# Kernel optimization log

Measured on AMD Instinct MI355X. Metric: run time of the kernel, lower is better.

## Reference

```python
import jax, jax.numpy as jnp
import numpy as np

V, T_BLOCK, D, H, L, HS = 32000, 1024, 1024, 16, 6, 64
B, T = 4, 1024
EPS = 1e-5


def setup_inputs() -> dict:
    key = jax.random.key(0)
    ks = jax.random.split(key, 12)
    s = 0.02  # init std, matches _init_weights
    return {
        'input_tokens': jax.random.randint(ks[0], (B, T), 0, V),
        'tok_emb': jax.random.normal(ks[1], (V, D), jnp.float32) * s,
        'pos_emb': jax.random.normal(ks[2], (T_BLOCK, D), jnp.float32) * s,
        'Wq': jax.random.normal(ks[3], (L, H, D, HS), jnp.float32) * s,
        'Wk': jax.random.normal(ks[4], (L, H, D, HS), jnp.float32) * s,
        'Wv': jax.random.normal(ks[5], (L, H, D, HS), jnp.float32) * s,
        'Wo': jax.random.normal(ks[6], (L, D, D), jnp.float32) * s,
        'bo': jnp.zeros((L, D), jnp.float32),
        'ln1_g': jnp.ones((L, D), jnp.float32),
        'ln1_b': jnp.zeros((L, D), jnp.float32),
        'ln2_g': jnp.ones((L, D), jnp.float32),
        'ln2_b': jnp.zeros((L, D), jnp.float32),
        'W1': jax.random.normal(ks[7], (L, D, 4 * D), jnp.float32) * s,
        'b1': jnp.zeros((L, 4 * D), jnp.float32),
        'W2': jax.random.normal(ks[8], (L, 4 * D, D), jnp.float32) * s,
        'b2': jnp.zeros((L, D), jnp.float32),
        'lnf_g': jnp.ones((D,), jnp.float32),
        'lnf_b': jnp.zeros((D,), jnp.float32),
        'W_out': jax.random.normal(ks[9], (D, V), jnp.float32) * s,
        'b_out': jnp.zeros((V,), jnp.float32),
    }


def _layer_norm(x, g, b):
    mu = jnp.mean(x, axis=-1, keepdims=True)
    var = jnp.mean(jnp.square(x - mu), axis=-1, keepdims=True)
    return (x - mu) * jax.lax.rsqrt(var + EPS) * g + b


def _attn(x, Wq, Wk, Wv, Wo, bo, causal_mask):
    # x: [B,T,D]; Wq/Wk/Wv: [H,D,hs] (per-head linears, bias=False)
    q = jnp.einsum('btd,hds->bhts', x, Wq)
    k = jnp.einsum('btd,hds->bhts', x, Wk)
    v = jnp.einsum('btd,hds->bhts', x, Wv)
    scores = jnp.einsum('bhts,bhus->bhtu', q, k) * (HS ** -0.5)
    scores = jnp.where(causal_mask, scores, -jnp.inf)
    w = jax.nn.softmax(scores, axis=-1)  # dropout=0.0 -> identity
    o = jnp.einsum('bhtu,bhus->bhts', w, v)
    # concat heads in order, then projection
    o = o.transpose(0, 2, 1, 3).reshape(x.shape[0], x.shape[1], H * HS)
    return o @ Wo + bo


def reference(input_tokens, tok_emb, pos_emb, Wq, Wk, Wv, Wo, bo,
              ln1_g, ln1_b, ln2_g, ln2_b, W1, b1, W2, b2,
              lnf_g, lnf_b, W_out, b_out):
    Bc, Tc = input_tokens.shape
    x = tok_emb[input_tokens] + pos_emb[:Tc]  # [B,T,D]
    mask = jnp.tril(jnp.ones((Tc, Tc), bool))[None, None]  # [1,1,T,T]
    for l in range(L):
        x = x + _attn(_layer_norm(x, ln1_g[l], ln1_b[l]),
                      Wq[l], Wk[l], Wv[l], Wo[l], bo[l], mask)
        h = _layer_norm(x, ln2_g[l], ln2_b[l])
        x = x + jax.nn.relu(h @ W1[l] + b1[l]) @ W2[l] + b2[l]
    x = _layer_norm(x, lnf_g, lnf_b)
    logits = x @ W_out + b_out  # [B,T,V]
    return logits
```

## Files before the change

kernel.cpp:

```cpp
#include <hip/hip_runtime.h>
#include <hip/hip_bf16.h>

#define HS 64
#define NH 16
#define DMODEL 1024
#define SEQ 1024
#define NB 4
#define NL 6
#define VOCAB 32000
#define EPS_LN 1e-5f

static constexpr int ROWS = NB * SEQ;

typedef float f32x4 __attribute__((ext_vector_type(4)));
typedef short bf16x8 __attribute__((ext_vector_type(8)));
typedef unsigned short u16x8 __attribute__((ext_vector_type(8)));
typedef unsigned short u16x4 __attribute__((ext_vector_type(4)));

__device__ __forceinline__ unsigned short f2b(float f) {
  __hip_bfloat16 h = __float2bfloat16(f);
  return *reinterpret_cast<unsigned short*>(&h);
}
__device__ __forceinline__ void gload_lds16(const void* g, void* l) {
  __builtin_amdgcn_global_load_lds(
      (const __attribute__((address_space(1))) void*)g,
      (__attribute__((address_space(3))) void*)l, 16, 0, 0);
}
#define MFMA16 __builtin_amdgcn_mfma_f32_16x16x32_bf16
#define EXP2F __builtin_amdgcn_exp2f

__global__ __launch_bounds__(256) void embed_kernel(
    const int* __restrict__ tokens, const float* __restrict__ tok_emb,
    const float* __restrict__ pos_emb, float* __restrict__ x) {
  int row = blockIdx.x;
  int t = row & (SEQ - 1);
  int tok = tokens[row];
  int d = threadIdx.x * 4;
  float4 te = *(const float4*)(tok_emb + (size_t)tok * DMODEL + d);
  float4 pe = *(const float4*)(pos_emb + (size_t)t * DMODEL + d);
  te.x += pe.x; te.y += pe.y; te.z += pe.z; te.w += pe.w;
  *(float4*)(x + (size_t)row * DMODEL + d) = te;
}

__global__ __launch_bounds__(256) void ln_kernel(
    const float* __restrict__ in, unsigned short* __restrict__ outp,
    const float* __restrict__ g, const float* __restrict__ b) {
  int row = blockIdx.x;
  int tid = threadIdx.x;
  const float* xr = in + (size_t)row * DMODEL;
  float4 v4 = *(const float4*)(xr + tid * 4);
  float s = v4.x + v4.y + v4.z + v4.w;
  float s2 = v4.x * v4.x + v4.y * v4.y + v4.z * v4.z + v4.w * v4.w;
#pragma unroll
  for (int off = 32; off > 0; off >>= 1) {
    s  += __shfl_down(s, off, 64);
    s2 += __shfl_down(s2, off, 64);
  }
  __shared__ float red[8];
  __shared__ float stats[2];
  int wv = tid >> 6, lane = tid & 63;
  if (lane == 0) { red[wv] = s; red[4 + wv] = s2; }
  __syncthreads();
  if (tid == 0) {
    float ts = red[0] + red[1] + red[2] + red[3];
    float ts2 = red[4] + red[5] + red[6] + red[7];
    float mu = ts * (1.0f / DMODEL);
    float var = ts2 * (1.0f / DMODEL) - mu * mu;
    stats[0] = mu;
    stats[1] = rsqrtf(var + EPS_LN);
  }
  __syncthreads();
  float mu = stats[0], rstd = stats[1];
  float4 g4 = *(const float4*)(g + tid * 4);
  float4 b4 = *(const float4*)(b + tid * 4);
  u16x4 o;
  o[0] = f2b((v4.x - mu) * rstd * g4.x + b4.x);
  o[1] = f2b((v4.y - mu) * rstd * g4.y + b4.y);
  o[2] = f2b((v4.z - mu) * rstd * g4.z + b4.z);
  o[3] = f2b((v4.w - mu) * rstd * g4.w + b4.w);
  *(u16x4*)(outp + (size_t)row * DMODEL + tid * 4) = o;
}

__global__ __launch_bounds__(256) void transconv(
    const float* __restrict__ in, unsigned short* __restrict__ outp, int K, int N) {
  __shared__ float tile[64][33];
  size_t zoff = (size_t)blockIdx.z * K * N;
  in += zoff;
  outp += zoff;
  int n0 = blockIdx.x * 32, k0 = blockIdx.y * 64;
  int tx = threadIdx.x & 31, ty = threadIdx.x >> 5;
#pragma unroll
  for (int i = 0; i < 8; ++i)
    tile[ty + i * 8][tx] = in[(size_t)(k0 + ty + i * 8) * N + n0 + tx];
  __syncthreads();
  int n = threadIdx.x >> 3;
  int kq = (threadIdx.x & 7) * 8;
  u16x8 o8;
#pragma unroll
  for (int j = 0; j < 8; ++j) o8[j] = f2b(tile[kq + j][n]);
  *(u16x8*)(outp + (size_t)(n0 + n) * K + k0 + kq) = o8;
}

__global__ __launch_bounds__(256) void qkv_transconv(
    const float* __restrict__ Wq, const float* __restrict__ Wk,
    const float* __restrict__ Wv, unsigned short* __restrict__ outp) {
  __shared__ float tile[64][33];
  int z = blockIdx.z;
  int l = z / 48;
  int r = z % 48;
  int which = r >> 4, h = r & 15;
  const float* W = (which == 0 ? Wq : which == 1 ? Wk : Wv) +
                   ((size_t)l * NH + h) * DMODEL * HS;
  int s0 = blockIdx.x * 32, d0 = blockIdx.y * 64;
  int tx = threadIdx.x & 31, ty = threadIdx.x >> 5;
#pragma unroll
  for (int i = 0; i < 8; ++i)
    tile[ty + i * 8][tx] = W[(size_t)(d0 + ty + i * 8) * HS + s0 + tx];
  __syncthreads();
  unsigned short* ob = outp + ((size_t)l * 3072 + which * 1024 + h * 64) * DMODEL;
  int n = threadIdx.x >> 3;
  int kq = (threadIdx.x & 7) * 8;
  u16x8 o8;
#pragma unroll
  for (int j = 0; j < 8; ++j) o8[j] = f2b(tile[kq + j][n]);
  *(u16x8*)(ob + (size_t)(s0 + n) * DMODEL + d0 + kq) = o8;
}

#define EPI_LOGITS 0
#define EPI_RES 1
#define EPI_RELU 2
#define EPI_QKV 3

template <int EPI, int BM_>
__global__ __launch_bounds__(512, 2) void mmX(
    const unsigned short* __restrict__ A, const unsigned short* __restrict__ Bt,
    const float* __restrict__ bias, const float* __restrict__ res,
    float* __restrict__ outf, unsigned short* __restrict__ ob0,
    unsigned short* __restrict__ ob1, unsigned short* __restrict__ ob2,
    int M, int N, int K) {
  constexpr int NA = BM_ / 64;
  constexpr int AP = BM_ / 128;
  constexpr int MFRAG = BM_ / 32;
  __shared__ __align__(16) unsigned short LDS[2][(BM_ + 256) * 64];
  const int tid = threadIdx.x;
  const int lane = tid & 63, w = tid >> 6;
  const int wm2 = w >> 2, wn4 = w & 3;
  const int l15 = lane & 15, l4 = lane >> 4;

  const int nM = M / BM_, nN = N >> 8;
  const int nwg = nM * nN;
  int bid = blockIdx.x;
  int wg = (bid & 7) * (nwg >> 3) + (bid >> 3);
  int mb = wg % nM, nb = wg / nM;
  const int m0 = mb * BM_, n0 = nb * 256;

  const int srow = tid >> 3;
  const int scolb = (tid & 7) * 16;
  const int swst = (srow & 7) << 4;
  const char* aS = (const char*)A + ((size_t)(m0 + srow) * K) * 2 + (scolb ^ swst);
  const char* bS = (const char*)Bt + ((size_t)(n0 + srow) * K) * 2 + (scolb ^ swst);
  const size_t rstep = (size_t)64 * K * 2;

  const int kb0 = l4 * 16;
  const int swz = (l15 & 7) << 4;

  const int NT = K >> 6;
  f32x4 acc[MFRAG][4] = {};
  bf16x8 bv[4][2], avA[AP][2], avB[AP][2];

#define STAGEX(tt)                                                          \
  {                                                                         \
    unsigned short* ad = &LDS[(tt) & 1][0] + (size_t)tid * 8;               \
    unsigned short* bd = &LDS[(tt) & 1][BM_ * 64] + (size_t)tid * 8;        \
    size_t ko = (size_t)(tt) * 128;                                         \
    _Pragma("unroll")                                                       \
    for (int j = 0; j < NA; ++j) gload_lds16(aS + ko + j * rstep, ad + j * 4096); \
    _Pragma("unroll")                                                       \
    for (int j = 0; j < 4; ++j) gload_lds16(bS + ko + j * rstep, bd + j * 4096);  \
  }

#define READA(dst, p)                                                       \
  _Pragma("unroll")                                                         \
  for (int mm = 0; mm < AP; ++mm)                                           \
  _Pragma("unroll")                                                         \
    for (int ks = 0; ks < 2; ++ks)                                          \
      dst[mm][ks] = *(const bf16x8*)(ab + (AP * (p) + mm) * 2048 +          \
                                     ((kb0 + 64 * ks) ^ swz));

#define GROUP(src, p)                                                       \
  __builtin_amdgcn_s_setprio(1);                                            \
  _Pragma("unroll")                                                         \
  for (int ks = 0; ks < 2; ++ks)                                            \
  _Pragma("unroll")                                                         \
    for (int mm = 0; mm < AP; ++mm)                                         \
    _Pragma("unroll")                                                       \
      for (int ni = 0; ni < 4; ++ni)                                        \
        acc[AP * (p) + mm][ni] =                                            \
            MFMA16(src[mm][ks], bv[ni][ks], acc[AP * (p) + mm][ni], 0, 0, 0);\
  __builtin_amdgcn_s_setprio(0);

  STAGEX(0)
  STAGEX(1)

  for (int t = 0; t < NT; ++t) {
    if (t < NT - 1) {
      if constexpr (BM_ == 256) asm volatile("s_waitcnt vmcnt(8)" ::: "memory");
      else                      asm volatile("s_waitcnt vmcnt(6)" ::: "memory");
    } else {
      asm volatile("s_waitcnt vmcnt(0)" ::: "memory");
    }
    __builtin_amdgcn_s_barrier();
    __builtin_amdgcn_sched_barrier(0);
    const char* ab = (const char*)&LDS[t & 1][0] +
                     (size_t)(wm2 * (BM_ / 2) + l15) * 128;
    const char* bb = (const char*)&LDS[t & 1][BM_ * 64] +
                     (size_t)(wn4 * 64 + l15) * 128;
#pragma unroll
    for (int ni = 0; ni < 4; ++ni)
#pragma unroll
      for (int ks = 0; ks < 2; ++ks)
        bv[ni][ks] = *(const bf16x8*)(bb + ni * 2048 + ((kb0 + 64 * ks) ^ swz));
    READA(avA, 0)
    READA(avB, 1)
    GROUP(avA, 0)
    READA(avA, 2)
    GROUP(avB, 1)
    READA(avB, 3)
    GROUP(avA, 2)
    asm volatile("s_waitcnt lgkmcnt(0)" ::: "memory");
    __builtin_amdgcn_sched_barrier(0);
    __builtin_amdgcn_s_barrier();
    __builtin_amdgcn_sched_barrier(0);
    if (t + 2 < NT) STAGEX(t + 2)
    GROUP(avB, 3)
  }
#undef STAGEX
#undef READA
#undef GROUP

  int rbase = m0 + wm2 * (BM_ / 2) + (l4 << 2);
  int cbase = n0 + wn4 * 64 + l15;

  if constexpr (EPI == EPI_LOGITS) {
    float* fl = (float*)&LDS[0][0];
#pragma unroll
    for (int half = 0; half < 2; ++half) {
      __syncthreads();
      if (wm2 == half) {
#pragma unroll
        for (int ni = 0; ni < 4; ++ni) {
          float bvv = bias[cbase + ni * 16];
          int cl = wn4 * 64 + l15 + ni * 16;
#pragma unroll
          for (int mi = 0; mi < MFRAG; ++mi) {
            int rl = mi * 16 + (l4 << 2);
#pragma unroll
            for (int r = 0; r < 4; ++r)
              fl[(rl + r) * 256 + cl] = acc[mi][ni][r] + bvv;
          }
        }
      }
      __syncthreads();
#pragma unroll
      for (int j = 0; j < 16; ++j) {
        int idx = j * 512 + tid;
        int rl = idx >> 6;
        int cc = (idx & 63) << 2;
        f32x4 v4 = *(const f32x4*)&fl[rl * 256 + cc];
        float* gp = outf + (size_t)(m0 + half * 128 + rl) * N + n0 + cc;
        __builtin_nontemporal_store(v4, (f32x4*)gp);
      }
    }
  } else {
#pragma unroll
    for (int ni = 0; ni < 4; ++ni) {
      int col = cbase + ni * 16;
      float bvv = 0.f;
      if (EPI != EPI_QKV) bvv = bias[col];
      if (EPI == EPI_QKV) {
        int which = col >> 10;
        int c2 = col & 1023;
        int h = c2 >> 6, s = c2 & 63;
#pragma unroll
        for (int mi = 0; mi < MFRAG; ++mi) {
          f32x4 a4 = acc[mi][ni];
          int row0 = rbase + mi * 16;
          int bb2 = row0 >> 10, t0 = row0 & 1023;
          if (which == 2) {
            u16x4 pk;
            pk[0] = f2b(a4[0]); pk[1] = f2b(a4[1]); pk[2] = f2b(a4[2]); pk[3] = f2b(a4[3]);
            *(u16x4*)(ob2 + ((((size_t)bb2 * NH + h) * HS) + s) * SEQ + t0) = pk;
          } else {
            unsigned short* dst = (which == 0) ? ob0 : ob1;
#pragma unroll
            for (int r = 0; r < 4; ++r)
              dst[((((size_t)bb2 * NH) + h) * SEQ + t0 + r) * HS + s] = f2b(a4[r]);
          }
        }
      } else {
#pragma unroll
        for (int mi = 0; mi < MFRAG; ++mi) {
          f32x4 a4 = acc[mi][ni];
#pragma unroll
          for (int r = 0; r < 4; ++r) {
            int rowg = rbase + mi * 16 + r;
            size_t off = (size_t)rowg * N + col;
            float v = a4[r] + bvv;
            if (EPI == EPI_RES) outf[off] = v + res[off];
            else if (EPI == EPI_RELU) ob0[off] = f2b(fmaxf(v, 0.f));
          }
        }
      }
    }
  }
}

template <int EPI>
__global__ __launch_bounds__(256, 2) void mmP(
    const unsigned short* __restrict__ A, const unsigned short* __restrict__ Bt,
    const float* __restrict__ bias, const float* __restrict__ res,
    float* __restrict__ outf, unsigned short* __restrict__ ob0,
    int M, int N, int K) {
  __shared__ __align__(16) unsigned short LDS[2][16384];
  const int tid = threadIdx.x;
  const int lane = tid & 63, w = tid >> 6;
  const int wm2 = w >> 1, wn2 = w & 1;
  const int l15 = lane & 15, l4 = lane >> 4;

  const int nM = M >> 7, nN = N >> 7;
  const int nwg = nM * nN;
  int bid = blockIdx.x;
  int wg = (bid & 7) * (nwg >> 3) + (bid >> 3);
  int mb = wg % nM, nb = wg / nM;
  const int m0 = mb * 128, n0 = nb * 128;

  const int srow = tid >> 3;
  const int scolb = (tid & 7) * 16;
  const int swst = (srow & 7) << 4;
  const char* aS = (const char*)A + ((size_t)(m0 + srow) * K) * 2 + (scolb ^ swst);
  const char* bS = (const char*)Bt + ((size_t)(n0 + srow) * K) * 2 + (scolb ^ swst);
  const size_t rstep = (size_t)32 * K * 2;

  const int kb0 = l4 * 16;
  const int swz = (l15 & 7) << 4;

  const int NT = K >> 6;
  f32x4 acc[4][4] = {};
  bf16x8 bv[4][2];

#define STAGEX(tt)                                                          \
  {                                                                         \
    unsigned short* ad = &LDS[(tt) & 1][0] + (size_t)tid * 8;               \
    unsigned short* bd = &LDS[(tt) & 1][8192] + (size_t)tid * 8;            \
    size_t ko = (size_t)(tt) * 128;                                         \
    _Pragma("unroll")                                                       \
    for (int j = 0; j < 4; ++j) gload_lds16(aS + ko + j * rstep, ad + j * 2048); \
    _Pragma("unroll")                                                       \
    for (int j = 0; j < 4; ++j) gload_lds16(bS + ko + j * rstep, bd + j * 2048); \
  }

#define RDA(dst, mi)                                                        \
  dst##k0 = *(const bf16x8*)(ab + (mi) * 2048 + (kb0 ^ swz));               \
  dst##k1 = *(const bf16x8*)(ab + (mi) * 2048 + ((kb0 + 64) ^ swz));

#define GROUP(src, mi)                                                      \
  __builtin_amdgcn_s_setprio(1);                                            \
  _Pragma("unroll")                                                         \
  for (int ni = 0; ni < 4; ++ni)                                            \
    acc[mi][ni] = MFMA16(src##k0, bv[ni][0], acc[mi][ni], 0, 0, 0);         \
  _Pragma("unroll")                                                         \
  for (int ni = 0; ni < 4; ++ni)                                            \
    acc[mi][ni] = MFMA16(src##k1, bv[ni][1], acc[mi][ni], 0, 0, 0);         \
  __builtin_amdgcn_s_setprio(0);

  STAGEX(0)
  STAGEX(1)

  for (int t = 0; t < NT; ++t) {
    if (t < NT - 1) asm volatile("s_waitcnt vmcnt(8)" ::: "memory");
    else            asm volatile("s_waitcnt vmcnt(0)" ::: "memory");
    __builtin_amdgcn_s_barrier();
    __builtin_amdgcn_sched_barrier(0);
    const char* ab = (const char*)&LDS[t & 1][0] + (size_t)(wm2 * 64 + l15) * 128;
    const char* bb = (const char*)&LDS[t & 1][8192] + (size_t)(wn2 * 64 + l15) * 128;
    bf16x8 aEk0, aEk1, aOk0, aOk1;
#pragma unroll
    for (int ni = 0; ni < 4; ++ni) {
      bv[ni][0] = *(const bf16x8*)(bb + ni * 2048 + (kb0 ^ swz));
      bv[ni][1] = *(const bf16x8*)(bb + ni * 2048 + ((kb0 + 64) ^ swz));
    }
    RDA(aE, 0)
    GROUP(aE, 0)
    RDA(aO, 1)
    GROUP(aO, 1)
    RDA(aE, 2)
    GROUP(aE, 2)
    RDA(aO, 3)
    asm volatile("s_waitcnt lgkmcnt(0)" ::: "memory");
    __builtin_amdgcn_sched_barrier(0);
    __builtin_amdgcn_s_barrier();
    __builtin_amdgcn_sched_barrier(0);
    if (t + 2 < NT) STAGEX(t + 2)
    GROUP(aO, 3)
  }
#undef STAGEX
#undef RDA
#undef GROUP

  int rbase = m0 + wm2 * 64 + (l4 << 2);
  int cbase = n0 + wn2 * 64 + l15;
#pragma unroll
  for (int ni = 0; ni < 4; ++ni) {
    int col = cbase + ni * 16;
    float bvv = bias[col];
#pragma unroll
    for (int mi = 0; mi < 4; ++mi) {
      f32x4 a4 = acc[mi][ni];
#pragma unroll
      for (int r = 0; r < 4; ++r) {
        int rowg = rbase + mi * 16 + r;
        size_t off = (size_t)rowg * N + col;
        float v = a4[r] + bvv;
        if (EPI == EPI_RES) outf[off] = v + res[off];
        else if (EPI == EPI_RELU) ob0[off] = f2b(fmaxf(v, 0.f));
      }
    }
  }
}

__global__ __launch_bounds__(256) void attn_mfma(
    const unsigned short* __restrict__ q, const unsigned short* __restrict__ k,
    const unsigned short* __restrict__ vt, unsigned short* __restrict__ outp) {
  __shared__ __align__(16) unsigned short S[32768];
  unsigned short* Ks = S;
  unsigned short* Vs = S + 16384;
  int qt = blockIdx.x, bh = blockIdx.y;
  int tid = threadIdx.x;
  int lane = tid & 63, w = tid >> 6;
  int l15 = lane & 15, l4 = lane >> 4;

  const unsigned short* qb = q + (size_t)bh * SEQ * HS;
  const unsigned short* kb = k + (size_t)bh * SEQ * HS;
  const unsigned short* vb = vt + (size_t)bh * HS * SEQ;

  int q_l = w * 16 + l15;
  int q_g = qt * 64 + q_l;
  bf16x8 qf[2];
  qf[0] = *(const bf16x8*)(qb + (size_t)q_g * HS + l4 * 8);
  qf[1] = *(const bf16x8*)(qb + (size_t)q_g * HS + l4 * 8 + 32);

  int kOff[4], vOff[4];
#pragma unroll
  for (int j = 0; j < 4; ++j) {
    int idx = tid + j * 256;
    kOff[j] = (idx >> 7) * 16 * HS + (idx & 15) * HS + ((idx >> 4) & 7) * 8;
    vOff[j] = ((idx >> 8) * 16 + (idx & 15)) * SEQ + ((idx >> 4) & 15) * 8;
  }

#define ASTAGE(tt)                                                           \
  {                                                                          \
    int bsel = ((tt) & 1) * 8192;                                            \
    const unsigned short* ksrc = kb + (size_t)(tt) * 128 * HS;               \
    const unsigned short* vsrc = vb + (tt) * 128;                            \
    _Pragma("unroll")                                                        \
    for (int j = 0; j < 4; ++j)                                              \
      gload_lds16(ksrc + kOff[j], Ks + bsel + (size_t)(tid + j * 256) * 8);  \
    _Pragma("unroll")                                                        \
    for (int j = 0; j < 4; ++j)                                              \
      gload_lds16(vsrc + vOff[j], Vs + bsel + (size_t)(tid + j * 256) * 8);  \
  }

  f32x4 o[4] = {};
  float mrun = -3e38f, lrun = 0.f;
  int baseLane = 32 * (l4 & 1) + l15;
  bool hi_t = (l4 >> 1) != 0;
  const float CSC = 0.125f * 1.44269504f;
  const float THR = 8.0f / CSC;

  int nt2 = (qt + 2) >> 1;
  ASTAGE(0)

  for (int kt = 0; kt < nt2; ++kt) {
    asm volatile("s_waitcnt vmcnt(0)" ::: "memory");
    __builtin_amdgcn_s_barrier();
    __builtin_amdgcn_sched_barrier(0);
    if (kt + 1 < nt2) ASTAGE(kt + 1)
    const unsigned short* Kb = Ks + (kt & 1) * 8192;
    const unsigned short* Vb = Vs + (kt & 1) * 8192;

    f32x4 s[8];
#pragma unroll
    for (int t = 0; t < 8; ++t) {
      bf16x8 kf0 = *(const bf16x8*)(Kb + ((size_t)(t * 8 + l4) * 16 + l15) * 8);
      bf16x8 kf1 = *(const bf16x8*)(Kb + ((size_t)(t * 8 + l4 + 4) * 16 + l15) * 8);
      s[t] = (f32x4){0.f, 0.f, 0.f, 0.f};
      s[t] = MFMA16(kf0, qf[0], s[t], 0, 0, 0);
      s[t] = MFMA16(kf1, qf[1], s[t], 0, 0, 0);
    }

    if (kt == nt2 - 1) {
      int keybase = kt * 128 + 4 * l4;
#pragma unroll
      for (int t = 0; t < 8; ++t)
#pragma unroll
        for (int r = 0; r < 4; ++r)
          if (keybase + 16 * t + r > q_g) s[t][r] = -3e38f;
    }
    float mx = -3e38f;
#pragma unroll
    for (int t = 0; t < 8; ++t)
#pragma unroll
      for (int r = 0; r < 4; ++r) mx = fmaxf(mx, s[t][r]);
    mx = fmaxf(mx, __shfl_xor(mx, 16, 64));
    mx = fmaxf(mx, __shfl_xor(mx, 32, 64));
    if (!__all(mx - mrun <= THR)) {
      float mnew = fmaxf(mrun, mx);
      float sc = EXP2F((mrun - mnew) * CSC);
      lrun *= sc;
#pragma unroll
      for (int t2 = 0; t2 < 4; ++t2)
#pragma unroll
        for (int r = 0; r < 4; ++r) o[t2][r] *= sc;
      mrun = mnew;
    }
    float mc = mrun * CSC;
    float ps = 0.f;
#pragma unroll
    for (int t = 0; t < 8; ++t)
#pragma unroll
      for (int r = 0; r < 4; ++r) {
        float e = EXP2F(__builtin_fmaf(s[t][r], CSC, -mc));
        s[t][r] = e;
        ps += e;
      }
    ps += __shfl_xor(ps, 16, 64);
    ps += __shfl_xor(ps, 32, 64);
    lrun += ps;

    int pd[8][2];
#pragma unroll
    for (int t = 0; t < 8; ++t)
#pragma unroll
      for (int h = 0; h < 2; ++h)
        pd[t][h] = (int)f2b(s[t][2 * h]) | ((int)f2b(s[t][2 * h + 1]) << 16);

#pragma unroll
    for (int kk = 0; kk < 4; ++kk) {
      int a0 = __shfl(pd[2 * kk][0], baseLane, 64);
      int b0 = __shfl(pd[2 * kk + 1][0], baseLane, 64);
      int a1 = __shfl(pd[2 * kk][1], baseLane, 64);
      int b1 = __shfl(pd[2 * kk + 1][1], baseLane, 64);
      int a2 = __shfl(pd[2 * kk][0], baseLane + 16, 64);
      int b2 = __shfl(pd[2 * kk + 1][0], baseLane + 16, 64);
      int a3 = __shfl(pd[2 * kk][1], baseLane + 16, 64);
      int b3 = __shfl(pd[2 * kk + 1][1], baseLane + 16, 64);
      union { int4 i4; bf16x8 v; } yu;
      yu.i4.x = hi_t ? b0 : a0;
      yu.i4.y = hi_t ? b1 : a1;
      yu.i4.z = hi_t ? b2 : a2;
      yu.i4.w = hi_t ? b3 : a3;
#pragma unroll
      for (int t2 = 0; t2 < 4; ++t2) {
        bf16x8 vf = *(const bf16x8*)(Vb + ((size_t)(t2 * 16 + kk * 4 + l4) * 16 + l15) * 8);
        o[t2] = MFMA16(vf, yu.v, o[t2], 0, 0, 0);
      }
    }
  }
#undef ASTAGE

  __syncthreads();
  float inv = 1.0f / lrun;
  unsigned short* Ol = S;
#pragma unroll
  for (int t2 = 0; t2 < 4; ++t2) {
    u16x4 p4;
#pragma unroll
    for (int r = 0; r < 4; ++r) p4[r] = f2b(o[t2][r] * inv);
    *(u16x4*)(Ol + (size_t)q_l * 72 + 16 * t2 + 4 * l4) = p4;
  }
  __syncthreads();
  int row = tid >> 2, hs0 = (tid & 3) * 16;
  int bidx = bh >> 4, h = bh & 15;
  size_t gbase = ((size_t)bidx * SEQ + qt * 64 + row) * DMODEL + h * HS + hs0;
  u16x8 r0 = *(const u16x8*)(Ol + (size_t)row * 72 + hs0);
  u16x8 r1 = *(const u16x8*)(Ol + (size_t)row * 72 + hs0 + 8);
  *(u16x8*)(outp + gbase) = r0;
  *(u16x8*)(outp + gbase + 8) = r1;
}

extern "C" void kernel_launch(void* const* d_in, const int* in_sizes, int n_in,
                              void* d_out, int out_size, void* d_ws, size_t ws_size,
                              hipStream_t stream) {
  const int*   tokens  = (const int*)d_in[0];
  const float* tok_emb = (const float*)d_in[1];
  const float* pos_emb = (const float*)d_in[2];
  const float* Wq      = (const float*)d_in[3];
  const float* Wk      = (const float*)d_in[4];
  const float* Wv      = (const float*)d_in[5];
  const float* Wo      = (const float*)d_in[6];
  const float* bo      = (const float*)d_in[7];
  const float* ln1_g   = (const float*)d_in[8];
  const float* ln1_b   = (const float*)d_in[9];
  const float* ln2_g   = (const float*)d_in[10];
  const float* ln2_b   = (const float*)d_in[11];
  const float* W1      = (const float*)d_in[12];
  const float* b1      = (const float*)d_in[13];
  const float* W2      = (const float*)d_in[14];
  const float* b2      = (const float*)d_in[15];
  const float* lnf_g   = (const float*)d_in[16];
  const float* lnf_b   = (const float*)d_in[17];
  const float* W_out   = (const float*)d_in[18];
  const float* b_out   = (const float*)d_in[19];
  float* logits = (float*)d_out;

  char* p = (char*)d_ws;
  float* x = (float*)p;            p += (size_t)ROWS * DMODEL * 4;
  unsigned short* hb = (unsigned short*)p;  p += (size_t)ROWS * DMODEL * 2;
  unsigned short* qb = (unsigned short*)p;  p += (size_t)ROWS * DMODEL * 2;
  unsigned short* kb = (unsigned short*)p;  p += (size_t)ROWS * DMODEL * 2;
  unsigned short* vtb = (unsigned short*)p; p += (size_t)ROWS * DMODEL * 2;
  unsigned short* att = (unsigned short*)p; p += (size_t)ROWS * DMODEL * 2;
  unsigned short* hid = (unsigned short*)p; p += (size_t)ROWS * 4 * DMODEL * 2;
  unsigned short* qkvt = (unsigned short*)p; p += (size_t)NL * 3 * DMODEL * DMODEL * 2;
  unsigned short* wot = (unsigned short*)p;  p += (size_t)NL * DMODEL * DMODEL * 2;
  unsigned short* w1t = (unsigned short*)p;  p += (size_t)NL * 4 * DMODEL * DMODEL * 2;
  unsigned short* w2t = (unsigned short*)p;  p += (size_t)NL * 4 * DMODEL * DMODEL * 2;
  unsigned short* woutt = (unsigned short*)p; p += (size_t)VOCAB * DMODEL * 2;

  transconv<<<dim3(32, 16, NL), 256, 0, stream>>>(Wo, wot, DMODEL, DMODEL);
  transconv<<<dim3(128, 16, NL), 256, 0, stream>>>(W1, w1t, DMODEL, 4 * DMODEL);
  transconv<<<dim3(32, 64, NL), 256, 0, stream>>>(W2, w2t, 4 * DMODEL, DMODEL);
  transconv<<<dim3(1000, 16, 1), 256, 0, stream>>>(W_out, woutt, DMODEL, VOCAB);
  qkv_transconv<<<dim3(2, 16, NL * 48), 256, 0, stream>>>(Wq, Wk, Wv, qkvt);

  embed_kernel<<<ROWS, 256, 0, stream>>>(tokens, tok_emb, pos_emb, x);

  for (int l = 0; l < NL; ++l) {
    ln_kernel<<<ROWS, 256, 0, stream>>>(x, hb, ln1_g + l * DMODEL, ln1_b + l * DMODEL);
    mmX<EPI_QKV, 128><<<384, 512, 0, stream>>>(
        hb, qkvt + (size_t)l * 3 * DMODEL * DMODEL, nullptr, nullptr,
        nullptr, qb, kb, vtb, ROWS, 3 * DMODEL, DMODEL);
    attn_mfma<<<dim3(SEQ / 64, NB * NH), 256, 0, stream>>>(qb, kb, vtb, att);
    mmP<EPI_RES><<<256, 256, 0, stream>>>(
        att, wot + (size_t)l * DMODEL * DMODEL, bo + l * DMODEL, x,
        x, nullptr, ROWS, DMODEL, DMODEL);
    ln_kernel<<<ROWS, 256, 0, stream>>>(x, hb, ln2_g + l * DMODEL, ln2_b + l * DMODEL);
    mmX<EPI_RELU, 256><<<256, 512, 0, stream>>>(
        hb, w1t + (size_t)l * 4 * DMODEL * DMODEL, b1 + (size_t)l * 4 * DMODEL, nullptr,
        nullptr, hid, nullptr, nullptr, ROWS, 4 * DMODEL, DMODEL);
    mmP<EPI_RES><<<256, 256, 0, stream>>>(
        hid, w2t + (size_t)l * 4 * DMODEL * DMODEL, b2 + l * DMODEL, x,
        x, nullptr, ROWS, DMODEL, 4 * DMODEL);
  }

  ln_kernel<<<ROWS, 256, 0, stream>>>(x, hb, lnf_g, lnf_b);
  mmX<EPI_LOGITS, 256><<<2000, 512, 0, stream>>>(
      hb, woutt, b_out, nullptr, logits, nullptr, nullptr, nullptr,
      ROWS, VOCAB, DMODEL);
}
```

Before: 1.776 ms.

## Replace 512-thread large-tile GEMM with 256-thread 64x256 tile kernel

```diff
diff --git a/kernel.cpp b/kernel.cpp
--- a/kernel.cpp
+++ b/kernel.cpp
@@ -131,145 +131,126 @@
 #define EPI_RELU 2
 #define EPI_QKV 3
 
-template <int EPI, int BM_>
-__global__ __launch_bounds__(512, 2) void mmX(
+template <int EPI>
+__global__ __launch_bounds__(256, 2) void mm64(
     const unsigned short* __restrict__ A, const unsigned short* __restrict__ Bt,
     const float* __restrict__ bias, const float* __restrict__ res,
     float* __restrict__ outf, unsigned short* __restrict__ ob0,
     unsigned short* __restrict__ ob1, unsigned short* __restrict__ ob2,
     int M, int N, int K) {
-  constexpr int NA = BM_ / 64;
-  constexpr int AP = BM_ / 128;
-  constexpr int MFRAG = BM_ / 32;
-  __shared__ __align__(16) unsigned short LDS[2][(BM_ + 256) * 64];
+  __shared__ __align__(16) unsigned short LDS[2][(64 + 256) * 64];
   const int tid = threadIdx.x;
-  const int lane = tid & 63, w = tid >> 6;
-  const int wm2 = w >> 2, wn4 = w & 3;
+  const int lane = tid & 63, wn4 = tid >> 6;
   const int l15 = lane & 15, l4 = lane >> 4;
 
-  const int nM = M / BM_, nN = N >> 8;
+  const int nM = M >> 6, nN = N >> 8;
   const int nwg = nM * nN;
   int bid = blockIdx.x;
   int wg = (bid & 7) * (nwg >> 3) + (bid >> 3);
   int mb = wg % nM, nb = wg / nM;
-  const int m0 = mb * BM_, n0 = nb * 256;
+  const int m0 = mb * 64, n0 = nb * 256;
 
   const int srow = tid >> 3;
   const int scolb = (tid & 7) * 16;
   const int swst = (srow & 7) << 4;
   const char* aS = (const char*)A + ((size_t)(m0 + srow) * K) * 2 + (scolb ^ swst);
   const char* bS = (const char*)Bt + ((size_t)(n0 + srow) * K) * 2 + (scolb ^ swst);
-  const size_t rstep = (size_t)64 * K * 2;
+  const size_t rstep = (size_t)32 * K * 2;
 
   const int kb0 = l4 * 16;
   const int swz = (l15 & 7) << 4;
 
   const int NT = K >> 6;
-  f32x4 acc[MFRAG][4] = {};
-  bf16x8 bv[4][2], avA[AP][2], avB[AP][2];
+  f32x4 acc[4][4] = {};
+  bf16x8 bv[4][2];
 
 #define STAGEX(tt)                                                          \
   {                                                                         \
     unsigned short* ad = &LDS[(tt) & 1][0] + (size_t)tid * 8;               \
-    unsigned short* bd = &LDS[(tt) & 1][BM_ * 64] + (size_t)tid * 8;        \
+    unsigned short* bd = &LDS[(tt) & 1][4096] + (size_t)tid * 8;            \
     size_t ko = (size_t)(tt) * 128;                                         \
     _Pragma("unroll")                                                       \
-    for (int j = 0; j < NA; ++j) gload_lds16(aS + ko + j * rstep, ad + j * 4096); \
+    for (int j = 0; j < 2; ++j) gload_lds16(aS + ko + j * rstep, ad + j * 2048); \
     _Pragma("unroll")                                                       \
-    for (int j = 0; j < 4; ++j) gload_lds16(bS + ko + j * rstep, bd + j * 4096);  \
-  }
-
-#define READA(dst, p)                                                       \
-  _Pragma("unroll")                                                         \
-  for (int mm = 0; mm < AP; ++mm)                                           \
-  _Pragma("unroll")                                                         \
-    for (int ks = 0; ks < 2; ++ks)                                          \
-      dst[mm][ks] = *(const bf16x8*)(ab + (AP * (p) + mm) * 2048 +          \
-                                     ((kb0 + 64 * ks) ^ swz));
-
-#define GROUP(src, p)                                                       \
+    for (int j = 0; j < 8; ++j) gload_lds16(bS + ko + j * rstep, bd + j * 2048); \
+  }
+
+#define RDA(dst, mi)                                                        \
+  dst##k0 = *(const bf16x8*)(ab + (mi) * 2048 + (kb0 ^ swz));               \
+  dst##k1 = *(const bf16x8*)(ab + (mi) * 2048 + ((kb0 + 64) ^ swz));
+
+#define GROUP(src, mi)                                                      \
   __builtin_amdgcn_s_setprio(1);                                            \
   _Pragma("unroll")                                                         \
-  for (int ks = 0; ks < 2; ++ks)                                            \
+  for (int ni = 0; ni < 4; ++ni)                                            \
+    acc[mi][ni] = MFMA16(src##k0, bv[ni][0], acc[mi][ni], 0, 0, 0);         \
   _Pragma("unroll")                                                         \
-    for (int mm = 0; mm < AP; ++mm)                                         \
-    _Pragma("unroll")                                                       \
-      for (int ni = 0; ni < 4; ++ni)                                        \
-        acc[AP * (p) + mm][ni] =                                            \
-            MFMA16(src[mm][ks], bv[ni][ks], acc[AP * (p) + mm][ni], 0, 0, 0);\
+  for (int ni = 0; ni < 4; ++ni)                                            \
+    acc[mi][ni] = MFMA16(src##k1, bv[ni][1], acc[mi][ni], 0, 0, 0);         \
   __builtin_amdgcn_s_setprio(0);
 
   STAGEX(0)
   STAGEX(1)
 
   for (int t = 0; t < NT; ++t) {
-    if (t < NT - 1) {
-      if constexpr (BM_ == 256) asm volatile("s_waitcnt vmcnt(8)" ::: "memory");
-      else                      asm volatile("s_waitcnt vmcnt(6)" ::: "memory");
-    } else {
-      asm volatile("s_waitcnt vmcnt(0)" ::: "memory");
-    }
+    if (t < NT - 1) asm volatile("s_waitcnt vmcnt(10)" ::: "memory");
+    else            asm volatile("s_waitcnt vmcnt(0)" ::: "memory");
     __builtin_amdgcn_s_barrier();
     __builtin_amdgcn_sched_barrier(0);
-    const char* ab = (const char*)&LDS[t & 1][0] +
-                     (size_t)(wm2 * (BM_ / 2) + l15) * 128;
-    const char* bb = (const char*)&LDS[t & 1][BM_ * 64] +
-                     (size_t)(wn4 * 64 + l15) * 128;
-#pragma unroll
-    for (int ni = 0; ni < 4; ++ni)
-#pragma unroll
-      for (int ks = 0; ks < 2; ++ks)
-        bv[ni][ks] = *(const bf16x8*)(bb + ni * 2048 + ((kb0 + 64 * ks) ^ swz));
-    READA(avA, 0)
-    READA(avB, 1)
-    GROUP(avA, 0)
-    READA(avA, 2)
-    GROUP(avB, 1)
-    READA(avB, 3)
-    GROUP(avA, 2)
+    const char* ab = (const char*)&LDS[t & 1][0] + (size_t)l15 * 128;
+    const char* bb = (const char*)&LDS[t & 1][4096] + (size_t)(wn4 * 64 + l15) * 128;
+    bf16x8 aEk0, aEk1, aOk0, aOk1;
+#pragma unroll
+    for (int ni = 0; ni < 4; ++ni) {
+      bv[ni][0] = *(const bf16x8*)(bb + ni * 2048 + (kb0 ^ swz));
+      bv[ni][1] = *(const bf16x8*)(bb + ni * 2048 + ((kb0 + 64) ^ swz));
+    }
+    RDA(aE, 0)
+    GROUP(aE, 0)
+    RDA(aO, 1)
+    GROUP(aO, 1)
+    RDA(aE, 2)
+    GROUP(aE, 2)
+    RDA(aO, 3)
     asm volatile("s_waitcnt lgkmcnt(0)" ::: "memory");
     __builtin_amdgcn_sched_barrier(0);
     __builtin_amdgcn_s_barrier();
     __builtin_amdgcn_sched_barrier(0);
     if (t + 2 < NT) STAGEX(t + 2)
-    GROUP(avB, 3)
+    GROUP(aO, 3)
   }
 #undef STAGEX
-#undef READA
+#undef RDA
 #undef GROUP
 
-  int rbase = m0 + wm2 * (BM_ / 2) + (l4 << 2);
+  int rbase = m0 + (l4 << 2);
   int cbase = n0 + wn4 * 64 + l15;
 
   if constexpr (EPI == EPI_LOGITS) {
     float* fl = (float*)&LDS[0][0];
-#pragma unroll
-    for (int half = 0; half < 2; ++half) {
-      __syncthreads();
-      if (wm2 == half) {
-#pragma unroll
-        for (int ni = 0; ni < 4; ++ni) {
-          float bvv = bias[cbase + ni * 16];
-          int cl = wn4 * 64 + l15 + ni * 16;
-#pragma unroll
-          for (int mi = 0; mi < MFRAG; ++mi) {
-            int rl = mi * 16 + (l4 << 2);
-#pragma unroll
-            for (int r = 0; r < 4; ++r)
-              fl[(rl + r) * 256 + cl] = acc[mi][ni][r] + bvv;
-          }
+    __syncthreads();
+#pragma unroll
+    for (int ni = 0; ni < 4; ++ni) {
+      float bvv = bias[cbase + ni * 16];
+      int cl = wn4 * 64 + l15 + ni * 16;
+#pragma unroll
+      for (int mi = 0; mi < 4; ++mi) {
+#pragma unroll
+        for (int r = 0; r < 4; ++r) {
+          int rl = mi * 16 + (l4 << 2) + r;
+          fl[rl * 260 + cl] = acc[mi][ni][r] + bvv;
         }
       }
-      __syncthreads();
-#pragma unroll
-      for (int j = 0; j < 16; ++j) {
-        int idx = j * 512 + tid;
-        int rl = idx >> 6;
-        int cc = (idx & 63) << 2;
-        f32x4 v4 = *(const f32x4*)&fl[rl * 256 + cc];
-        float* gp = outf + (size_t)(m0 + half * 128 + rl) * N + n0 + cc;
-        __builtin_nontemporal_store(v4, (f32x4*)gp);
-      }
+    }
+    __syncthreads();
+#pragma unroll
+    for (int j = 0; j < 16; ++j) {
+      int idx = j * 256 + tid;
+      int rl = idx >> 6;
+      int cc = (idx & 63) << 2;
+      f32x4 v4 = *(const f32x4*)&fl[rl * 260 + cc];
+      float* gp = outf + (size_t)(m0 + rl) * N + n0 + cc;
+      __builtin_nontemporal_store(v4, (f32x4*)gp);
     }
   } else {
 #pragma unroll
@@ -282,7 +263,7 @@
         int c2 = col & 1023;
         int h = c2 >> 6, s = c2 & 63;
 #pragma unroll
-        for (int mi = 0; mi < MFRAG; ++mi) {
+        for (int mi = 0; mi < 4; ++mi) {
           f32x4 a4 = acc[mi][ni];
           int row0 = rbase + mi * 16;
           int bb2 = row0 >> 10, t0 = row0 & 1023;
@@ -299,7 +280,7 @@
         }
       } else {
 #pragma unroll
-        for (int mi = 0; mi < MFRAG; ++mi) {
+        for (int mi = 0; mi < 4; ++mi) {
           f32x4 a4 = acc[mi][ni];
 #pragma unroll
           for (int r = 0; r < 4; ++r) {
@@ -637,7 +618,7 @@
 
   for (int l = 0; l < NL; ++l) {
     ln_kernel<<<ROWS, 256, 0, stream>>>(x, hb, ln1_g + l * DMODEL, ln1_b + l * DMODEL);
-    mmX<EPI_QKV, 128><<<384, 512, 0, stream>>>(
+    mm64<EPI_QKV><<<768, 256, 0, stream>>>(
         hb, qkvt + (size_t)l * 3 * DMODEL * DMODEL, nullptr, nullptr,
         nullptr, qb, kb, vtb, ROWS, 3 * DMODEL, DMODEL);
     attn_mfma<<<dim3(SEQ / 64, NB * NH), 256, 0, stream>>>(qb, kb, vtb, att);
@@ -645,7 +626,7 @@
         att, wot + (size_t)l * DMODEL * DMODEL, bo + l * DMODEL, x,
         x, nullptr, ROWS, DMODEL, DMODEL);
     ln_kernel<<<ROWS, 256, 0, stream>>>(x, hb, ln2_g + l * DMODEL, ln2_b + l * DMODEL);
-    mmX<EPI_RELU, 256><<<256, 512, 0, stream>>>(
+    mm64<EPI_RELU><<<1024, 256, 0, stream>>>(
         hb, w1t + (size_t)l * 4 * DMODEL * DMODEL, b1 + (size_t)l * 4 * DMODEL, nullptr,
         nullptr, hid, nullptr, nullptr, ROWS, 4 * DMODEL, DMODEL);
     mmP<EPI_RES><<<256, 256, 0, stream>>>(
@@ -654,7 +635,7 @@
   }
 
   ln_kernel<<<ROWS, 256, 0, stream>>>(x, hb, lnf_g, lnf_b);
-  mmX<EPI_LOGITS, 256><<<2000, 512, 0, stream>>>(
+  mm64<EPI_LOGITS><<<8000, 256, 0, stream>>>(
       hb, woutt, b_out, nullptr, logits, nullptr, nullptr, nullptr,
       ROWS, VOCAB, DMODEL);
 }
```

New measurement: 1.834 ms. 1.03x slower.
